# Optimization experiments

Measured on AMD Instinct MI355X. Metric: run time of the kernel, lower is better.

Reference implementation:

```python
import jax, jax.numpy as jnp
import numpy as np

B = 65536
IN_DIM = 512
H0, H1 = 256, 128
HEAD_H = 64
D = 12
K_MAX = 3
EPS = 1e-5
# predecessor indices per disease (topologically ordered DAG)
PRED_LISTS = [[], [0], [0], [1, 2], [0, 3], [2], [4, 5], [1, 6], [3, 7], [6, 8], [5, 9], [8, 10, 9]]


def setup_inputs() -> dict:
    key = jax.random.key(0)
    ks = jax.random.split(key, 16)
    x = jax.random.normal(ks[0], (B, IN_DIM), jnp.float32)
    enc_W0 = jax.random.normal(ks[1], (IN_DIM, H0), jnp.float32) * 0.04
    enc_b0 = jnp.zeros((H0,), jnp.float32)
    bn0_g = jnp.ones((H0,), jnp.float32)
    bn0_b = jnp.zeros((H0,), jnp.float32)
    bn0_m = jax.random.normal(ks[2], (H0,), jnp.float32) * 0.1
    bn0_v = jax.random.uniform(ks[3], (H0,), jnp.float32, 0.5, 1.5)
    enc_W1 = jax.random.normal(ks[4], (H0, H1), jnp.float32) * 0.06
    enc_b1 = jnp.zeros((H1,), jnp.float32)
    bn1_g = jnp.ones((H1,), jnp.float32)
    bn1_b = jnp.zeros((H1,), jnp.float32)
    bn1_m = jax.random.normal(ks[5], (H1,), jnp.float32) * 0.1
    bn1_v = jax.random.uniform(ks[6], (H1,), jnp.float32, 0.5, 1.5)
    w_init = jax.random.normal(ks[7], (D, H1), jnp.float32) * 0.09   # head.layer1 (pass-1 logit)
    b_init = jnp.zeros((D,), jnp.float32)
    Wz = jax.random.normal(ks[8], (D, H1, HEAD_H), jnp.float32) * 0.09   # head first layer, z-columns
    Wp = jax.random.normal(ks[9], (D, K_MAX, HEAD_H), jnp.float32) * 0.09  # head first layer, predecessor columns (padded)
    bh = jnp.zeros((D, HEAD_H), jnp.float32)
    Wo = jax.random.normal(ks[10], (D, HEAD_H), jnp.float32) * 0.12
    bo = jnp.zeros((D,), jnp.float32)
    idx = np.zeros((D, K_MAX), np.int32)
    w = np.zeros((D, K_MAX), np.float32)
    for d, preds in enumerate(PRED_LISTS):
        for j, p in enumerate(preds):
            idx[d, j] = p
            w[d, j] = 0.5  # DAG edge weight; zero entries are padding
    return {"x": x, "enc_W0": enc_W0, "enc_b0": enc_b0, "bn0_g": bn0_g, "bn0_b": bn0_b,
            "bn0_m": bn0_m, "bn0_v": bn0_v, "enc_W1": enc_W1, "enc_b1": enc_b1,
            "bn1_g": bn1_g, "bn1_b": bn1_b, "bn1_m": bn1_m, "bn1_v": bn1_v,
            "w_init": w_init, "b_init": b_init, "Wz": Wz, "Wp": Wp, "bh": bh,
            "Wo": Wo, "bo": bo, "pred_w": jnp.asarray(w), "pred_idx": jnp.asarray(idx)}


def reference(x, enc_W0, enc_b0, bn0_g, bn0_b, bn0_m, bn0_v, enc_W1, enc_b1,
              bn1_g, bn1_b, bn1_m, bn1_v, w_init, b_init, Wz, Wp, bh, Wo, bo,
              pred_w, pred_idx):
    # Shared encoder: Linear -> BatchNorm(eval stats) -> ReLU, twice (dropout identity at eval)
    h = x @ enc_W0 + enc_b0
    h = jax.nn.relu((h - bn0_m) * jax.lax.rsqrt(bn0_v + EPS) * bn0_g + bn0_b)
    z = h @ enc_W1 + enc_b1
    z = jax.nn.relu((z - bn1_m) * jax.lax.rsqrt(bn1_v + EPS) * bn1_g + bn1_b)  # [B, H1]
    # Pass 1: initial per-disease prediction = sigmoid(head.layer1(z))
    p = jax.nn.sigmoid(z @ w_init.T + b_init)  # [B, D]
    # Pass 2: DAG gather of predecessor predictions, edge-weighted; padding slots have weight 0
    aug = p[:, pred_idx] * pred_w  # [B, D, K_MAX]
    # Per-disease head: Linear(H1 + k -> HEAD_H) split into z-part + predecessor-part, ReLU, Linear(HEAD_H -> 1), sigmoid
    hid = jax.nn.relu(jnp.einsum('be,deh->bdh', z, Wz) + jnp.einsum('bdk,dkh->bdh', aug, Wp) + bh)
    out = jax.nn.sigmoid(jnp.einsum('bdh,dh->bd', hid, Wo) + bo)  # [B, D] = torch.cat of final_preds
    return out
```

## Files before the change

kernel.cpp:

```cpp
#include <hip/hip_runtime.h>

#define B_TOT   65536
#define IN_DIM  512
#define H0      256
#define H1      128
#define HH      64
#define NDIS    12

typedef __bf16 bf16_t;
typedef __bf16 bf16x4 __attribute__((ext_vector_type(4)));
typedef __bf16 bf16x8 __attribute__((ext_vector_type(8)));
typedef float  f32x4  __attribute__((ext_vector_type(4)));
typedef float  floatx4 __attribute__((ext_vector_type(4)));

#define WS_W0T   0u
#define WS_W1T   262144u
#define WS_WZT   327680u
#define WS_WIT   524288u
#define WS_AL0   528384u
#define WS_BE0   529408u
#define WS_AL1   530432u
#define WS_BE1   530944u
#define WS_Z     531456u
#define WS_NEED  (531456u + 16777216u)

__global__ void prep_kernel(const float* __restrict__ W0, const float* __restrict__ b0,
                            const float* __restrict__ g0, const float* __restrict__ bb0,
                            const float* __restrict__ mm0, const float* __restrict__ vv0,
                            const float* __restrict__ W1, const float* __restrict__ b1,
                            const float* __restrict__ g1, const float* __restrict__ bb1,
                            const float* __restrict__ mm1, const float* __restrict__ vv1,
                            const float* __restrict__ w_init, const float* __restrict__ Wz,
                            char* __restrict__ ws)
{
    bf16_t* W0t = (bf16_t*)(ws + WS_W0T);
    bf16_t* W1t = (bf16_t*)(ws + WS_W1T);
    bf16_t* Wzt = (bf16_t*)(ws + WS_WZT);
    bf16_t* wiT = (bf16_t*)(ws + WS_WIT);
    float* al0 = (float*)(ws + WS_AL0);
    float* be0 = (float*)(ws + WS_BE0);
    float* al1 = (float*)(ws + WS_AL1);
    float* be1 = (float*)(ws + WS_BE1);

    int t = blockIdx.x * 256 + threadIdx.x;

    {
        int c = t >> 9, k = t & 511;
        W0t[t] = (bf16_t)W0[k * H0 + c];
    }
    if (t < H1 * H0) {
        int c = t >> 8, k = t & 255;
        W1t[t] = (bf16_t)W1[k * H1 + c];
    }
    if (t < NDIS * HH * H1) {
        int d = t >> 13, r = t & 8191, h = r >> 7, e = r & 127;
        Wzt[t] = (bf16_t)Wz[d * 8192 + e * 64 + h];
    }
    if (t < 16 * H1) {
        int d = t >> 7, e = t & 127;
        wiT[t] = (d < NDIS) ? (bf16_t)w_init[d * H1 + e] : (bf16_t)0.0f;
    }
    if (t < H0) {
        float a = g0[t] * rsqrtf(vv0[t] + 1e-5f);
        al0[t] = a;
        be0[t] = (b0[t] - mm0[t]) * a + bb0[t];
    }
    if (t < H1) {
        float a = g1[t] * rsqrtf(vv1[t] + 1e-5f);
        al1[t] = a;
        be1[t] = (b1[t] - mm1[t]) * a + bb1[t];
    }
}

__global__ __launch_bounds__(512, 4) void enc_kernel(
    const float* __restrict__ x,
    const bf16_t* __restrict__ W0t, const bf16_t* __restrict__ W1t,
    const float* __restrict__ al0, const float* __restrict__ be0,
    const float* __restrict__ al1, const float* __restrict__ be1,
    bf16_t* __restrict__ z_ws)
{
    __shared__ __align__(16) char smem[46080];
    bf16_t* xs  = (bf16_t*)smem;
    bf16_t* w0s = (bf16_t*)(smem + 9216);
    bf16_t* hs  = (bf16_t*)smem;

    const int tid  = threadIdx.x;
    const int lane = tid & 63, wid = tid >> 6;
    const int wr = wid >> 2, wc = wid & 3;
    const int l15 = lane & 15, lg = lane >> 4;
    const int m0 = blockIdx.x * 64;

    f32x4 acc[2][4] = {};
    for (int ks = 0; ks < 8; ++ks) {
        #pragma unroll
        for (int i = 0; i < 2; ++i) {
            int flat = i * 512 + tid;
            int row = flat >> 4, c4 = (flat & 15) << 2;
            floatx4 v = *(const floatx4*)(x + (m0 + row) * IN_DIM + ks * 64 + c4);
            bf16x4 o;
            o[0] = (bf16_t)v[0]; o[1] = (bf16_t)v[1];
            o[2] = (bf16_t)v[2]; o[3] = (bf16_t)v[3];
            *(bf16x4*)(xs + row * 72 + c4) = o;
        }
        #pragma unroll
        for (int i = 0; i < 4; ++i) {
            int flat = i * 512 + tid;
            int c = flat >> 3, k8 = (flat & 7) << 3;
            *(bf16x8*)(w0s + c * 72 + k8) = *(const bf16x8*)(W0t + c * IN_DIM + ks * 64 + k8);
        }
        __syncthreads();
        #pragma unroll
        for (int kf = 0; kf < 2; ++kf) {
            bf16x8 a[2], b[4];
            #pragma unroll
            for (int mr = 0; mr < 2; ++mr)
                a[mr] = *(const bf16x8*)(xs + (wr * 32 + mr * 16 + l15) * 72 + kf * 32 + lg * 8);
            #pragma unroll
            for (int nr = 0; nr < 4; ++nr)
                b[nr] = *(const bf16x8*)(w0s + (wc * 64 + nr * 16 + l15) * 72 + kf * 32 + lg * 8);
            #pragma unroll
            for (int mr = 0; mr < 2; ++mr)
                #pragma unroll
                for (int nr = 0; nr < 4; ++nr)
                    acc[mr][nr] = __builtin_amdgcn_mfma_f32_16x16x32_bf16(a[mr], b[nr], acc[mr][nr], 0, 0, 0);
        }
        __syncthreads();
    }

    #pragma unroll
    for (int mr = 0; mr < 2; ++mr)
        #pragma unroll
        for (int nr = 0; nr < 4; ++nr) {
            int c = wc * 64 + nr * 16 + l15;
            float alpha = al0[c], beta = be0[c];
            #pragma unroll
            for (int j = 0; j < 4; ++j) {
                int r = wr * 32 + mr * 16 + lg * 4 + j;
                float v = fmaxf(acc[mr][nr][j] * alpha + beta, 0.0f);
                hs[r * 264 + c] = (bf16_t)v;
            }
        }
    __syncthreads();

    f32x4 acc2[2][2] = {};
    #pragma unroll
    for (int kf = 0; kf < 8; ++kf) {
        bf16x8 a[2], b[2];
        #pragma unroll
        for (int mr = 0; mr < 2; ++mr)
            a[mr] = *(const bf16x8*)(hs + (wr * 32 + mr * 16 + l15) * 264 + kf * 32 + lg * 8);
        #pragma unroll
        for (int nr = 0; nr < 2; ++nr) {
            int c = wc * 32 + nr * 16 + l15;
            b[nr] = *(const bf16x8*)(W1t + c * H0 + kf * 32 + lg * 8);
        }
        #pragma unroll
        for (int mr = 0; mr < 2; ++mr)
            #pragma unroll
            for (int nr = 0; nr < 2; ++nr)
                acc2[mr][nr] = __builtin_amdgcn_mfma_f32_16x16x32_bf16(a[mr], b[nr], acc2[mr][nr], 0, 0, 0);
    }

    #pragma unroll
    for (int mr = 0; mr < 2; ++mr)
        #pragma unroll
        for (int nr = 0; nr < 2; ++nr) {
            int c = wc * 32 + nr * 16 + l15;
            float alpha = al1[c], beta = be1[c];
            #pragma unroll
            for (int j = 0; j < 4; ++j) {
                int r = wr * 32 + mr * 16 + lg * 4 + j;
                float v = fmaxf(acc2[mr][nr][j] * alpha + beta, 0.0f);
                z_ws[(m0 + r) * H1 + c] = (bf16_t)v;
            }
        }
}

__global__ __launch_bounds__(512, 4) void head_kernel(
    const bf16_t* __restrict__ z_ws,
    const bf16_t* __restrict__ Wzt, const bf16_t* __restrict__ wiT,
    const float* __restrict__ b_init, const float* __restrict__ Wp,
    const float* __restrict__ bh, const float* __restrict__ Wo,
    const float* __restrict__ bo, const float* __restrict__ pred_w,
    const int* __restrict__ pred_idx, float* __restrict__ out)
{
    __shared__ __align__(16) char smem[64768];
    bf16_t* zs  = (bf16_t*)smem;
    bf16_t* wis = (bf16_t*)(smem + 34816);
    float*  ps  = (float*)(smem + 34816 + 4352);
    bf16_t* wzs = (bf16_t*)(smem + 34816 + 4352 + 8192);

    const int tid  = threadIdx.x;
    const int lane = tid & 63, wid = tid >> 6;
    const int l15 = lane & 15, lg = lane >> 4;
    const int m0 = blockIdx.x * 128;

    #pragma unroll
    for (int i = 0; i < 4; ++i) {
        int flat = i * 512 + tid;
        int row = flat >> 4, k8 = (flat & 15) << 3;
        *(bf16x8*)(zs + row * 136 + k8) = *(const bf16x8*)(z_ws + (m0 + row) * H1 + k8);
    }
    if (tid < 256) {
        int row = tid >> 4, k8 = (tid & 15) << 3;
        *(bf16x8*)(wis + row * 136 + k8) = *(const bf16x8*)(wiT + row * H1 + k8);
    }
    __syncthreads();

    {
        f32x4 pacc = {};
        #pragma unroll
        for (int kf = 0; kf < 4; ++kf) {
            bf16x8 a = *(const bf16x8*)(zs + (wid * 16 + l15) * 136 + kf * 32 + lg * 8);
            bf16x8 b = *(const bf16x8*)(wis + l15 * 136 + kf * 32 + lg * 8);
            pacc = __builtin_amdgcn_mfma_f32_16x16x32_bf16(a, b, pacc, 0, 0, 0);
        }
        int d = l15;
        float bi = (d < NDIS) ? b_init[d] : 0.0f;
        #pragma unroll
        for (int j = 0; j < 4; ++j) {
            int r = wid * 16 + lg * 4 + j;
            ps[r * 16 + d] = 1.0f / (1.0f + __expf(-(pacc[j] + bi)));
        }
    }
    __syncthreads();

    for (int d = 0; d < NDIS; ++d) {
        #pragma unroll
        for (int i = 0; i < 2; ++i) {
            int flat = i * 512 + tid;
            int row = flat >> 4, k8 = (flat & 15) << 3;
            *(bf16x8*)(wzs + row * 136 + k8) = *(const bf16x8*)(Wzt + d * 8192 + row * H1 + k8);
        }
        __syncthreads();

        f32x4 acc[4] = {};
        #pragma unroll
        for (int kf = 0; kf < 4; ++kf) {
            bf16x8 a = *(const bf16x8*)(zs + (wid * 16 + l15) * 136 + kf * 32 + lg * 8);
            #pragma unroll
            for (int nr = 0; nr < 4; ++nr) {
                bf16x8 b = *(const bf16x8*)(wzs + (nr * 16 + l15) * 136 + kf * 32 + lg * 8);
                acc[nr] = __builtin_amdgcn_mfma_f32_16x16x32_bf16(a, b, acc[nr], 0, 0, 0);
            }
        }

        int i0 = pred_idx[d * 3 + 0], i1 = pred_idx[d * 3 + 1], i2 = pred_idx[d * 3 + 2];
        float w0p = pred_w[d * 3 + 0], w1p = pred_w[d * 3 + 1], w2p = pred_w[d * 3 + 2];
        float bod = bo[d];

        float aug0[4], aug1[4], aug2[4];
        #pragma unroll
        for (int j = 0; j < 4; ++j) {
            int r = wid * 16 + lg * 4 + j;
            aug0[j] = ps[r * 16 + i0] * w0p;
            aug1[j] = ps[r * 16 + i1] * w1p;
            aug2[j] = ps[r * 16 + i2] * w2p;
        }
        float res[4] = {0.f, 0.f, 0.f, 0.f};
        #pragma unroll
        for (int nr = 0; nr < 4; ++nr) {
            int c = nr * 16 + l15;
            float bhv = bh[d * 64 + c];
            float wp0 = Wp[d * 192 + c], wp1 = Wp[d * 192 + 64 + c], wp2 = Wp[d * 192 + 128 + c];
            float wov = Wo[d * 64 + c];
            #pragma unroll
            for (int j = 0; j < 4; ++j) {
                float v = acc[nr][j] + bhv + aug0[j] * wp0 + aug1[j] * wp1 + aug2[j] * wp2;
                res[j] += fmaxf(v, 0.0f) * wov;
            }
        }
        #pragma unroll
        for (int j = 0; j < 4; ++j) {
            float s = res[j];
            s += __shfl_xor(s, 1); s += __shfl_xor(s, 2);
            s += __shfl_xor(s, 4); s += __shfl_xor(s, 8);
            if (l15 == 0) {
                int r = wid * 16 + lg * 4 + j;
                out[(m0 + r) * NDIS + d] = 1.0f / (1.0f + __expf(-(s + bod)));
            }
        }
        __syncthreads();
    }
}

extern "C" void kernel_launch(void* const* d_in, const int* in_sizes, int n_in,
                              void* d_out, int out_size, void* d_ws, size_t ws_size,
                              hipStream_t stream) {
    if (ws_size < (size_t)WS_NEED) return;

    const float* x      = (const float*)d_in[0];
    const float* W0     = (const float*)d_in[1];
    const float* b0     = (const float*)d_in[2];
    const float* g0     = (const float*)d_in[3];
    const float* bb0    = (const float*)d_in[4];
    const float* mm0    = (const float*)d_in[5];
    const float* vv0    = (const float*)d_in[6];
    const float* W1     = (const float*)d_in[7];
    const float* b1     = (const float*)d_in[8];
    const float* g1     = (const float*)d_in[9];
    const float* bb1    = (const float*)d_in[10];
    const float* mm1    = (const float*)d_in[11];
    const float* vv1    = (const float*)d_in[12];
    const float* w_init = (const float*)d_in[13];
    const float* b_init = (const float*)d_in[14];
    const float* Wz     = (const float*)d_in[15];
    const float* Wp     = (const float*)d_in[16];
    const float* bh     = (const float*)d_in[17];
    const float* Wo     = (const float*)d_in[18];
    const float* bo     = (const float*)d_in[19];
    const float* pred_w = (const float*)d_in[20];
    const int*   pred_idx = (const int*)d_in[21];

    char* ws = (char*)d_ws;
    bf16_t* W0t = (bf16_t*)(ws + WS_W0T);
    bf16_t* W1t = (bf16_t*)(ws + WS_W1T);
    bf16_t* Wzt = (bf16_t*)(ws + WS_WZT);
    bf16_t* wiT = (bf16_t*)(ws + WS_WIT);
    float* al0 = (float*)(ws + WS_AL0);
    float* be0 = (float*)(ws + WS_BE0);
    float* al1 = (float*)(ws + WS_AL1);
    float* be1 = (float*)(ws + WS_BE1);
    bf16_t* z_ws = (bf16_t*)(ws + WS_Z);

    prep_kernel<<<dim3(512), dim3(256), 0, stream>>>(
        W0, b0, g0, bb0, mm0, vv0, W1, b1, g1, bb1, mm1, vv1, w_init, Wz, ws);

    enc_kernel<<<dim3(B_TOT / 64), dim3(512), 0, stream>>>(
        x, W0t, W1t, al0, be0, al1, be1, z_ws);

    head_kernel<<<dim3(B_TOT / 128), dim3(512), 0, stream>>>(
        z_ws, Wzt, wiT, b_init, Wp, bh, Wo, bo, pred_w, pred_idx, (float*)d_out);
}
```

Before: 95.14 us.

## Fuse encoder and head kernels with register-prefetched double-buffered layer-0 loop

Merges the encoder and per-disease head into one kernel, so the bf16 z activations stay in shared memory and no longer make a 16 MB global round trip. The layer-0 K loop now uses a 32-wide K step with double-buffered LDS and register prefetch, overlapping global loads with MFMA work. The head phase splits the 8 waves into two groups that each handle 6 diseases on 64 rows. In exchange, each block does more serial work and occupancy drops from 4 to 3 blocks, and the head phase reloads the Wz weights per 64-row block rather than per 128.

```diff
diff --git a/kernel.cpp b/kernel.cpp
--- a/kernel.cpp
+++ b/kernel.cpp
@@ -21,8 +21,18 @@
 #define WS_BE0   529408u
 #define WS_AL1   530432u
 #define WS_BE1   530944u
-#define WS_Z     531456u
-#define WS_NEED  (531456u + 16777216u)
+#define WS_NEED  531456u
+
+#define L_XS0    0u
+#define L_W0S0   5120u
+#define L_XS1    25600u
+#define L_W0S1   30720u
+#define L_HS     0u
+#define L_WZS    0u
+#define L_ZS     34816u
+#define L_PS     52224u
+#define L_WIS    56320u
+#define L_TOTAL  60672u
 
 __global__ void prep_kernel(const float* __restrict__ W0, const float* __restrict__ b0,
                             const float* __restrict__ g0, const float* __restrict__ bb0,
@@ -72,215 +82,237 @@
     }
 }
 
-__global__ __launch_bounds__(512, 4) void enc_kernel(
+__global__ __launch_bounds__(512, 3) void fused_kernel(
     const float* __restrict__ x,
     const bf16_t* __restrict__ W0t, const bf16_t* __restrict__ W1t,
     const float* __restrict__ al0, const float* __restrict__ be0,
     const float* __restrict__ al1, const float* __restrict__ be1,
-    bf16_t* __restrict__ z_ws)
-{
-    __shared__ __align__(16) char smem[46080];
-    bf16_t* xs  = (bf16_t*)smem;
-    bf16_t* w0s = (bf16_t*)(smem + 9216);
-    bf16_t* hs  = (bf16_t*)smem;
-
-    const int tid  = threadIdx.x;
-    const int lane = tid & 63, wid = tid >> 6;
-    const int wr = wid >> 2, wc = wid & 3;
-    const int l15 = lane & 15, lg = lane >> 4;
-    const int m0 = blockIdx.x * 64;
-
-    f32x4 acc[2][4] = {};
-    for (int ks = 0; ks < 8; ++ks) {
-        #pragma unroll
-        for (int i = 0; i < 2; ++i) {
-            int flat = i * 512 + tid;
-            int row = flat >> 4, c4 = (flat & 15) << 2;
-            floatx4 v = *(const floatx4*)(x + (m0 + row) * IN_DIM + ks * 64 + c4);
-            bf16x4 o;
-            o[0] = (bf16_t)v[0]; o[1] = (bf16_t)v[1];
-            o[2] = (bf16_t)v[2]; o[3] = (bf16_t)v[3];
-            *(bf16x4*)(xs + row * 72 + c4) = o;
-        }
-        #pragma unroll
-        for (int i = 0; i < 4; ++i) {
-            int flat = i * 512 + tid;
-            int c = flat >> 3, k8 = (flat & 7) << 3;
-            *(bf16x8*)(w0s + c * 72 + k8) = *(const bf16x8*)(W0t + c * IN_DIM + ks * 64 + k8);
-        }
-        __syncthreads();
-        #pragma unroll
-        for (int kf = 0; kf < 2; ++kf) {
-            bf16x8 a[2], b[4];
-            #pragma unroll
-            for (int mr = 0; mr < 2; ++mr)
-                a[mr] = *(const bf16x8*)(xs + (wr * 32 + mr * 16 + l15) * 72 + kf * 32 + lg * 8);
-            #pragma unroll
-            for (int nr = 0; nr < 4; ++nr)
-                b[nr] = *(const bf16x8*)(w0s + (wc * 64 + nr * 16 + l15) * 72 + kf * 32 + lg * 8);
-            #pragma unroll
-            for (int mr = 0; mr < 2; ++mr)
-                #pragma unroll
-                for (int nr = 0; nr < 4; ++nr)
-                    acc[mr][nr] = __builtin_amdgcn_mfma_f32_16x16x32_bf16(a[mr], b[nr], acc[mr][nr], 0, 0, 0);
-        }
-        __syncthreads();
-    }
-
-    #pragma unroll
-    for (int mr = 0; mr < 2; ++mr)
-        #pragma unroll
-        for (int nr = 0; nr < 4; ++nr) {
-            int c = wc * 64 + nr * 16 + l15;
-            float alpha = al0[c], beta = be0[c];
-            #pragma unroll
-            for (int j = 0; j < 4; ++j) {
-                int r = wr * 32 + mr * 16 + lg * 4 + j;
-                float v = fmaxf(acc[mr][nr][j] * alpha + beta, 0.0f);
-                hs[r * 264 + c] = (bf16_t)v;
-            }
-        }
-    __syncthreads();
-
-    f32x4 acc2[2][2] = {};
-    #pragma unroll
-    for (int kf = 0; kf < 8; ++kf) {
-        bf16x8 a[2], b[2];
-        #pragma unroll
-        for (int mr = 0; mr < 2; ++mr)
-            a[mr] = *(const bf16x8*)(hs + (wr * 32 + mr * 16 + l15) * 264 + kf * 32 + lg * 8);
-        #pragma unroll
-        for (int nr = 0; nr < 2; ++nr) {
-            int c = wc * 32 + nr * 16 + l15;
-            b[nr] = *(const bf16x8*)(W1t + c * H0 + kf * 32 + lg * 8);
-        }
-        #pragma unroll
-        for (int mr = 0; mr < 2; ++mr)
-            #pragma unroll
-            for (int nr = 0; nr < 2; ++nr)
-                acc2[mr][nr] = __builtin_amdgcn_mfma_f32_16x16x32_bf16(a[mr], b[nr], acc2[mr][nr], 0, 0, 0);
-    }
-
-    #pragma unroll
-    for (int mr = 0; mr < 2; ++mr)
-        #pragma unroll
-        for (int nr = 0; nr < 2; ++nr) {
-            int c = wc * 32 + nr * 16 + l15;
-            float alpha = al1[c], beta = be1[c];
-            #pragma unroll
-            for (int j = 0; j < 4; ++j) {
-                int r = wr * 32 + mr * 16 + lg * 4 + j;
-                float v = fmaxf(acc2[mr][nr][j] * alpha + beta, 0.0f);
-                z_ws[(m0 + r) * H1 + c] = (bf16_t)v;
-            }
-        }
-}
-
-__global__ __launch_bounds__(512, 4) void head_kernel(
-    const bf16_t* __restrict__ z_ws,
     const bf16_t* __restrict__ Wzt, const bf16_t* __restrict__ wiT,
     const float* __restrict__ b_init, const float* __restrict__ Wp,
     const float* __restrict__ bh, const float* __restrict__ Wo,
     const float* __restrict__ bo, const float* __restrict__ pred_w,
     const int* __restrict__ pred_idx, float* __restrict__ out)
 {
-    __shared__ __align__(16) char smem[64768];
-    bf16_t* zs  = (bf16_t*)smem;
-    bf16_t* wis = (bf16_t*)(smem + 34816);
-    float*  ps  = (float*)(smem + 34816 + 4352);
-    bf16_t* wzs = (bf16_t*)(smem + 34816 + 4352 + 8192);
+    __shared__ __align__(16) char smem[L_TOTAL];
 
     const int tid  = threadIdx.x;
     const int lane = tid & 63, wid = tid >> 6;
     const int l15 = lane & 15, lg = lane >> 4;
-    const int m0 = blockIdx.x * 128;
+    const int m0 = blockIdx.x * 64;
+
+    {
+        bf16_t* wis = (bf16_t*)(smem + L_WIS);
+        if (tid < 256) {
+            int row = tid >> 4, k8 = (tid & 15) << 3;
+            *(bf16x8*)(wis + row * 136 + k8) = *(const bf16x8*)(wiT + row * H1 + k8);
+        }
+    }
+
+    const int wr = wid >> 2, wc = wid & 3;
+    const int xrow = tid >> 3, xc4 = (tid & 7) << 2;
+    const int wrow = tid >> 2, wk8 = (tid & 3) << 3;
+    const float*  xp  = x + (m0 + xrow) * IN_DIM + xc4;
+    const bf16_t* wp0 = W0t + wrow * IN_DIM + wk8;
+    const bf16_t* wp1 = W0t + (wrow + 128) * IN_DIM + wk8;
+
+    bf16_t* xsb[2]  = { (bf16_t*)(smem + L_XS0),  (bf16_t*)(smem + L_XS1)  };
+    bf16_t* w0sb[2] = { (bf16_t*)(smem + L_W0S0), (bf16_t*)(smem + L_W0S1) };
+
+    floatx4 xvA, xvB;
+    bf16x8  wvA0, wvA1, wvB0, wvB1;
+
+#define LOAD_A(ks) { xvA = *(const floatx4*)(xp + (ks) * 32); \
+                     wvA0 = *(const bf16x8*)(wp0 + (ks) * 32); \
+                     wvA1 = *(const bf16x8*)(wp1 + (ks) * 32); }
+#define LOAD_B(ks) { xvB = *(const floatx4*)(xp + (ks) * 32); \
+                     wvB0 = *(const bf16x8*)(wp0 + (ks) * 32); \
+                     wvB1 = *(const bf16x8*)(wp1 + (ks) * 32); }
+#define STORE_A(bi) { bf16x4 xo; xo[0]=(bf16_t)xvA[0]; xo[1]=(bf16_t)xvA[1]; \
+                      xo[2]=(bf16_t)xvA[2]; xo[3]=(bf16_t)xvA[3]; \
+                      *(bf16x4*)(xsb[bi] + xrow * 40 + xc4) = xo; \
+                      *(bf16x8*)(w0sb[bi] + wrow * 40 + wk8) = wvA0; \
+                      *(bf16x8*)(w0sb[bi] + (wrow + 128) * 40 + wk8) = wvA1; }
+#define STORE_B(bi) { bf16x4 xo; xo[0]=(bf16_t)xvB[0]; xo[1]=(bf16_t)xvB[1]; \
+                      xo[2]=(bf16_t)xvB[2]; xo[3]=(bf16_t)xvB[3]; \
+                      *(bf16x4*)(xsb[bi] + xrow * 40 + xc4) = xo; \
+                      *(bf16x8*)(w0sb[bi] + wrow * 40 + wk8) = wvB0; \
+                      *(bf16x8*)(w0sb[bi] + (wrow + 128) * 40 + wk8) = wvB1; }
+
+    f32x4 acc[2][4] = {};
+#define MFMA_STEP(bi) { bf16x8 a[2], b[4]; \
+    _Pragma("unroll") \
+    for (int mr = 0; mr < 2; ++mr) \
+        a[mr] = *(const bf16x8*)(xsb[bi] + (wr * 32 + mr * 16 + l15) * 40 + lg * 8); \
+    _Pragma("unroll") \
+    for (int nr = 0; nr < 4; ++nr) \
+        b[nr] = *(const bf16x8*)(w0sb[bi] + (wc * 64 + nr * 16 + l15) * 40 + lg * 8); \
+    _Pragma("unroll") \
+    for (int mr = 0; mr < 2; ++mr) \
+        _Pragma("unroll") \
+        for (int nr = 0; nr < 4; ++nr) \
+            acc[mr][nr] = __builtin_amdgcn_mfma_f32_16x16x32_bf16(a[mr], b[nr], acc[mr][nr], 0, 0, 0); }
+
+    LOAD_A(0);
+    STORE_A(0);
+    LOAD_B(1);
+    __syncthreads();
 
     #pragma unroll
-    for (int i = 0; i < 4; ++i) {
-        int flat = i * 512 + tid;
-        int row = flat >> 4, k8 = (flat & 15) << 3;
-        *(bf16x8*)(zs + row * 136 + k8) = *(const bf16x8*)(z_ws + (m0 + row) * H1 + k8);
-    }
-    if (tid < 256) {
-        int row = tid >> 4, k8 = (tid & 15) << 3;
-        *(bf16x8*)(wis + row * 136 + k8) = *(const bf16x8*)(wiT + row * H1 + k8);
+    for (int tt = 0; tt < 8; ++tt) {
+        if (tt < 7) LOAD_A(2 * tt + 2);
+        MFMA_STEP(0);
+        STORE_B(1);
+        __syncthreads();
+        if (tt < 7) LOAD_B(2 * tt + 3);
+        MFMA_STEP(1);
+        if (tt < 7) STORE_A(0);
+        __syncthreads();
+    }
+
+    {
+        bf16_t* hs = (bf16_t*)(smem + L_HS);
+        #pragma unroll
+        for (int mr = 0; mr < 2; ++mr)
+            #pragma unroll
+            for (int nr = 0; nr < 4; ++nr) {
+                int c = wc * 64 + nr * 16 + l15;
+                float alpha = al0[c], beta = be0[c];
+                #pragma unroll
+                for (int j = 0; j < 4; ++j) {
+                    int r = wr * 32 + mr * 16 + lg * 4 + j;
+                    float v = fmaxf(acc[mr][nr][j] * alpha + beta, 0.0f);
+                    hs[r * 264 + c] = (bf16_t)v;
+                }
+            }
     }
     __syncthreads();
 
     {
-        f32x4 pacc = {};
+        bf16_t* hs = (bf16_t*)(smem + L_HS);
+        bf16_t* zs = (bf16_t*)(smem + L_ZS);
+        f32x4 acc2[2][2] = {};
         #pragma unroll
-        for (int kf = 0; kf < 4; ++kf) {
-            bf16x8 a = *(const bf16x8*)(zs + (wid * 16 + l15) * 136 + kf * 32 + lg * 8);
-            bf16x8 b = *(const bf16x8*)(wis + l15 * 136 + kf * 32 + lg * 8);
-            pacc = __builtin_amdgcn_mfma_f32_16x16x32_bf16(a, b, pacc, 0, 0, 0);
-        }
-        int d = l15;
-        float bi = (d < NDIS) ? b_init[d] : 0.0f;
-        #pragma unroll
-        for (int j = 0; j < 4; ++j) {
-            int r = wid * 16 + lg * 4 + j;
-            ps[r * 16 + d] = 1.0f / (1.0f + __expf(-(pacc[j] + bi)));
-        }
-    }
-    __syncthreads();
-
-    for (int d = 0; d < NDIS; ++d) {
-        #pragma unroll
-        for (int i = 0; i < 2; ++i) {
-            int flat = i * 512 + tid;
-            int row = flat >> 4, k8 = (flat & 15) << 3;
-            *(bf16x8*)(wzs + row * 136 + k8) = *(const bf16x8*)(Wzt + d * 8192 + row * H1 + k8);
-        }
-        __syncthreads();
-
-        f32x4 acc[4] = {};
-        #pragma unroll
-        for (int kf = 0; kf < 4; ++kf) {
-            bf16x8 a = *(const bf16x8*)(zs + (wid * 16 + l15) * 136 + kf * 32 + lg * 8);
-            #pragma unroll
-            for (int nr = 0; nr < 4; ++nr) {
-                bf16x8 b = *(const bf16x8*)(wzs + (nr * 16 + l15) * 136 + kf * 32 + lg * 8);
-                acc[nr] = __builtin_amdgcn_mfma_f32_16x16x32_bf16(a, b, acc[nr], 0, 0, 0);
-            }
-        }
-
-        int i0 = pred_idx[d * 3 + 0], i1 = pred_idx[d * 3 + 1], i2 = pred_idx[d * 3 + 2];
-        float w0p = pred_w[d * 3 + 0], w1p = pred_w[d * 3 + 1], w2p = pred_w[d * 3 + 2];
-        float bod = bo[d];
-
-        float aug0[4], aug1[4], aug2[4];
-        #pragma unroll
-        for (int j = 0; j < 4; ++j) {
-            int r = wid * 16 + lg * 4 + j;
-            aug0[j] = ps[r * 16 + i0] * w0p;
-            aug1[j] = ps[r * 16 + i1] * w1p;
-            aug2[j] = ps[r * 16 + i2] * w2p;
-        }
-        float res[4] = {0.f, 0.f, 0.f, 0.f};
-        #pragma unroll
-        for (int nr = 0; nr < 4; ++nr) {
-            int c = nr * 16 + l15;
-            float bhv = bh[d * 64 + c];
-            float wp0 = Wp[d * 192 + c], wp1 = Wp[d * 192 + 64 + c], wp2 = Wp[d * 192 + 128 + c];
-            float wov = Wo[d * 64 + c];
-            #pragma unroll
-            for (int j = 0; j < 4; ++j) {
-                float v = acc[nr][j] + bhv + aug0[j] * wp0 + aug1[j] * wp1 + aug2[j] * wp2;
-                res[j] += fmaxf(v, 0.0f) * wov;
-            }
+        for (int kf = 0; kf < 8; ++kf) {
+            bf16x8 a[2], b[2];
+            #pragma unroll
+            for (int mr = 0; mr < 2; ++mr)
+                a[mr] = *(const bf16x8*)(hs + (wr * 32 + mr * 16 + l15) * 264 + kf * 32 + lg * 8);
+            #pragma unroll
+            for (int nr = 0; nr < 2; ++nr) {
+                int c = wc * 32 + nr * 16 + l15;
+                b[nr] = *(const bf16x8*)(W1t + c * H0 + kf * 32 + lg * 8);
+            }
+            #pragma unroll
+            for (int mr = 0; mr < 2; ++mr)
+                #pragma unroll
+                for (int nr = 0; nr < 2; ++nr)
+                    acc2[mr][nr] = __builtin_amdgcn_mfma_f32_16x16x32_bf16(a[mr], b[nr], acc2[mr][nr], 0, 0, 0);
         }
         #pragma unroll
-        for (int j = 0; j < 4; ++j) {
-            float s = res[j];
-            s += __shfl_xor(s, 1); s += __shfl_xor(s, 2);
-            s += __shfl_xor(s, 4); s += __shfl_xor(s, 8);
-            if (l15 == 0) {
+        for (int mr = 0; mr < 2; ++mr)
+            #pragma unroll
+            for (int nr = 0; nr < 2; ++nr) {
+                int c = wc * 32 + nr * 16 + l15;
+                float alpha = al1[c], beta = be1[c];
+                #pragma unroll
+                for (int j = 0; j < 4; ++j) {
+                    int r = wr * 32 + mr * 16 + lg * 4 + j;
+                    float v = fmaxf(acc2[mr][nr][j] * alpha + beta, 0.0f);
+                    zs[r * 136 + c] = (bf16_t)v;
+                }
+            }
+    }
+    __syncthreads();
+
+    {
+        bf16_t* zs  = (bf16_t*)(smem + L_ZS);
+        bf16_t* wis = (bf16_t*)(smem + L_WIS);
+        float*  ps  = (float*)(smem + L_PS);
+        if (wid < 4) {
+            f32x4 pacc = {};
+            #pragma unroll
+            for (int kf = 0; kf < 4; ++kf) {
+                bf16x8 a = *(const bf16x8*)(zs + (wid * 16 + l15) * 136 + kf * 32 + lg * 8);
+                bf16x8 b = *(const bf16x8*)(wis + l15 * 136 + kf * 32 + lg * 8);
+                pacc = __builtin_amdgcn_mfma_f32_16x16x32_bf16(a, b, pacc, 0, 0, 0);
+            }
+            int d = l15;
+            float bi = (d < NDIS) ? b_init[d] : 0.0f;
+            #pragma unroll
+            for (int j = 0; j < 4; ++j) {
                 int r = wid * 16 + lg * 4 + j;
-                out[(m0 + r) * NDIS + d] = 1.0f / (1.0f + __expf(-(s + bod)));
+                ps[r * 16 + d] = 1.0f / (1.0f + __expf(-(pacc[j] + bi)));
             }
         }
-        __syncthreads();
+    }
+    __syncthreads();
+
+    {
+        bf16_t* zs  = (bf16_t*)(smem + L_ZS);
+        float*  ps  = (float*)(smem + L_PS);
+        const int g  = wid >> 2;
+        const int mt = wid & 3;
+        const int lt = tid & 255;
+        bf16_t* wzs = (bf16_t*)(smem + L_WZS) + g * 8704;
+
+        for (int i = 0; i < 6; ++i) {
+            int d = g * 6 + i;
+            #pragma unroll
+            for (int j = 0; j < 4; ++j) {
+                int chunk = j * 256 + lt;
+                int row = chunk >> 4, k8 = (chunk & 15) << 3;
+                *(bf16x8*)(wzs + row * 136 + k8) = *(const bf16x8*)(Wzt + d * 8192 + row * H1 + k8);
+            }
+            __syncthreads();
+
+            f32x4 hacc[4] = {};
+            #pragma unroll
+            for (int kf = 0; kf < 4; ++kf) {
+                bf16x8 a = *(const bf16x8*)(zs + (mt * 16 + l15) * 136 + kf * 32 + lg * 8);
+                #pragma unroll
+                for (int nr = 0; nr < 4; ++nr) {
+                    bf16x8 b = *(const bf16x8*)(wzs + (nr * 16 + l15) * 136 + kf * 32 + lg * 8);
+                    hacc[nr] = __builtin_amdgcn_mfma_f32_16x16x32_bf16(a, b, hacc[nr], 0, 0, 0);
+                }
+            }
+
+            int i0 = pred_idx[d * 3 + 0], i1 = pred_idx[d * 3 + 1], i2 = pred_idx[d * 3 + 2];
+            float w0p = pred_w[d * 3 + 0], w1p = pred_w[d * 3 + 1], w2p = pred_w[d * 3 + 2];
+            float bod = bo[d];
+
+            float aug0[4], aug1[4], aug2[4];
+            #pragma unroll
+            for (int j = 0; j < 4; ++j) {
+                int r = mt * 16 + lg * 4 + j;
+                aug0[j] = ps[r * 16 + i0] * w0p;
+                aug1[j] = ps[r * 16 + i1] * w1p;
+                aug2[j] = ps[r * 16 + i2] * w2p;
+            }
+            float res[4] = {0.f, 0.f, 0.f, 0.f};
+            #pragma unroll
+            for (int nr = 0; nr < 4; ++nr) {
+                int c = nr * 16 + l15;
+                float bhv = bh[d * 64 + c];
+                float wpa = Wp[d * 192 + c], wpb = Wp[d * 192 + 64 + c], wpc = Wp[d * 192 + 128 + c];
+                float wov = Wo[d * 64 + c];
+                #pragma unroll
+                for (int j = 0; j < 4; ++j) {
+                    float v = hacc[nr][j] + bhv + aug0[j] * wpa + aug1[j] * wpb + aug2[j] * wpc;
+                    res[j] += fmaxf(v, 0.0f) * wov;
+                }
+            }
+            #pragma unroll
+            for (int j = 0; j < 4; ++j) {
+                float s = res[j];
+                s += __shfl_xor(s, 1); s += __shfl_xor(s, 2);
+                s += __shfl_xor(s, 4); s += __shfl_xor(s, 8);
+                if (l15 == 0) {
+                    int r = mt * 16 + lg * 4 + j;
+                    out[(m0 + r) * NDIS + d] = 1.0f / (1.0f + __expf(-(s + bod)));
+                }
+            }
+            __syncthreads();
+        }
     }
 }
 
@@ -300,8 +332,8 @@
     const float* b1     = (const float*)d_in[8];
     const float* g1     = (const float*)d_in[9];
     const float* bb1    = (const float*)d_in[10];
+    const float* vv1_   = (const float*)d_in[12];
     const float* mm1    = (const float*)d_in[11];
-    const float* vv1    = (const float*)d_in[12];
     const float* w_init = (const float*)d_in[13];
     const float* b_init = (const float*)d_in[14];
     const float* Wz     = (const float*)d_in[15];
@@ -313,22 +345,19 @@
     const int*   pred_idx = (const int*)d_in[21];
 
     char* ws = (char*)d_ws;
-    bf16_t* W0t = (bf16_t*)(ws + WS_W0T);
-    bf16_t* W1t = (bf16_t*)(ws + WS_W1T);
-    bf16_t* Wzt = (bf16_t*)(ws + WS_WZT);
-    bf16_t* wiT = (bf16_t*)(ws + WS_WIT);
-    float* al0 = (float*)(ws + WS_AL0);
-    float* be0 = (float*)(ws + WS_BE0);
-    float* al1 = (float*)(ws + WS_AL1);
-    float* be1 = (float*)(ws + WS_BE1);
-    bf16_t* z_ws = (bf16_t*)(ws + WS_Z);
+    const bf16_t* W0t = (const bf16_t*)(ws + WS_W0T);
+    const bf16_t* W1t = (const bf16_t*)(ws + WS_W1T);
+    const bf16_t* Wzt = (const bf16_t*)(ws + WS_WZT);
+    const bf16_t* wiT = (const bf16_t*)(ws + WS_WIT);
+    const float* al0 = (const float*)(ws + WS_AL0);
+    const float* be0 = (const float*)(ws + WS_BE0);
+    const float* al1 = (const float*)(ws + WS_AL1);
+    const float* be1 = (const float*)(ws + WS_BE1);
 
     prep_kernel<<<dim3(512), dim3(256), 0, stream>>>(
-        W0, b0, g0, bb0, mm0, vv0, W1, b1, g1, bb1, mm1, vv1, w_init, Wz, ws);
-
-    enc_kernel<<<dim3(B_TOT / 64), dim3(512), 0, stream>>>(
-        x, W0t, W1t, al0, be0, al1, be1, z_ws);
-
-    head_kernel<<<dim3(B_TOT / 128), dim3(512), 0, stream>>>(
-        z_ws, Wzt, wiT, b_init, Wp, bh, Wo, bo, pred_w, pred_idx, (float*)d_out);
+        W0, b0, g0, bb0, mm0, vv0, W1, b1, g1, bb1, mm1, vv1_, w_init, Wz, ws);
+
+    fused_kernel<<<dim3(B_TOT / 64), dim3(512), 0, stream>>>(
+        x, W0t, W1t, al0, be0, al1, be1, Wzt, wiT, b_init, Wp, bh, Wo, bo,
+        pred_w, pred_idx, (float*)d_out);
 }
```

Result: faster. 91.33 us (-4.0%).
